# Performance work log

Hardware: AMD Instinct MI355X
Metric: run time of the kernel (lower is better)

Reference implementation:

```python
import jax, jax.numpy as jnp
import numpy as np

EPS = 1e-7  # keras.backend.epsilon()


def setup_inputs() -> dict:
    key = jax.random.key(0)
    k1, k2, k3 = jax.random.split(key, 3)
    B, N, D_in, C, D_out = 32, 2048, 8, 32, 16
    x = jax.random.normal(k1, (B, N, D_in), dtype=jnp.float32)
    W = jax.random.normal(k2, (1, N, C, D_out, D_in), dtype=jnp.float32) * 0.05
    R = jax.random.normal(k3, (1, N, C), dtype=jnp.float32)
    return {"x": x, "W": W, "R": R}


def reference(x, W, R):
    # x: [B, N, D_in]; W: [1, N, C, D_out, D_in]; R: [1, N, C]
    R_nor = jax.nn.softmax(R[0], axis=0)          # softmax over N (axis=1 of [1,N,C])
    # per-capsule transform: u[b,n,c,j] = sum_k W[n,c,j,k] * x[b,n,k]
    u = jnp.einsum('ncjk,bnk->bncj', W[0], x)
    # routing-weighted aggregation over input capsules n
    s = jnp.einsum('bncj,nc->bcj', u, R_nor)      # [B, C, D_out]
    # squash along capsule dim (original axis=-2 before squeeze == D_out)
    ss = jnp.sum(jnp.square(s), axis=-1, keepdims=True) + EPS
    scale = jnp.sqrt(ss) / (1.0 + ss)
    return scale * s                               # [B, C, D_out]
```

## Files before the change

### kernel.cpp

```cpp
#include <hip/hip_runtime.h>
#include <math.h>


#define NN 2048
#define CC 32

__device__ __forceinline__ void g2l16(const float* g, float* l) {
  __builtin_amdgcn_global_load_lds((const __attribute__((address_space(1))) void*)g,
                                   (__attribute__((address_space(3))) void*)l, 16, 0, 0);
}

__global__ void __launch_bounds__(512) caps_main(const float* __restrict__ x,
                                                 const float* __restrict__ W,
                                                 const float* __restrict__ R,
                                                 float* __restrict__ P) {
  const int bid = blockIdx.x;
  const int cq = bid >> 6;
  const int chunk = bid & 63;
  const int n0 = chunk * 32;
  const int tid = threadIdx.x;
  const int ws = tid >> 6;
  const int lane = tid & 63;
  const int j = lane & 15;
  const int bo = lane >> 4;

  extern __shared__ float smem[];
  float* ldsW = smem;
  float* ldsX = smem + 8192;
  float* red8 = smem + 4096;

#pragma unroll
  for (int it = 0; it < 2; ++it) {
    int idx = it * 512 + tid;
    int nl = idx >> 7, S = idx & 127;
    int g = S ^ (((S >> 2) ^ (S >> 4)) & 1) ^ (((S >> 3) & 1) << 1) ^ (((S >> 4) & 1) << 2);
    g2l16(W + (size_t)(n0 + nl) * 4096 + cq * 512 + g * 4,
          ldsW + (size_t)(it * 512 + ws * 64) * 4);
  }

  float4 xg[4];
  int xoff[4];
#pragma unroll
  for (int it = 0; it < 4; ++it) {
    int idx = it * 512 + tid;
    int nl = idx >> 6, r = idx & 63;
    int b = r & 31, kq = r >> 5;
    xg[it] = *(const float4*)(x + (size_t)b * (NN * 8) + (size_t)(n0 + nl) * 8 + kq * 4);
    xoff[it] = nl * 256 + kq * 128 + b;
  }
#pragma unroll
  for (int it = 0; it < 4; ++it) {
    float* d = ldsX + xoff[it];
    d[0] = xg[it].x; d[32] = xg[it].y; d[64] = xg[it].z; d[96] = xg[it].w;
  }

  float se[4] = {0.f, 0.f, 0.f, 0.f};
#pragma unroll
  for (int i = 0; i < 4; ++i) {
    int n = i * 512 + tid;
    float4 a = *(const float4*)(R + (size_t)n * CC + cq * 4);
    se[0] += expf(a.x); se[1] += expf(a.y); se[2] += expf(a.z); se[3] += expf(a.w);
  }
#pragma unroll
  for (int ci = 0; ci < 4; ++ci) {
    float v = se[ci];
#pragma unroll
    for (int d = 32; d >= 1; d >>= 1) v += __shfl_xor(v, d, 64);
    se[ci] = v;
  }
  if (lane == 0) {
#pragma unroll
    for (int ci = 0; ci < 4; ++ci) red8[ws * 4 + ci] = se[ci];
  }
  __syncthreads();

  float inv4[4];
  {
    float t[4] = {0.f, 0.f, 0.f, 0.f};
#pragma unroll
    for (int w = 0; w < 8; ++w)
#pragma unroll
      for (int ci = 0; ci < 4; ++ci) t[ci] += red8[w * 4 + ci];
#pragma unroll
    for (int ci = 0; ci < 4; ++ci) inv4[ci] = 1.0f / t[ci];
  }
  __syncthreads();

  float acc[4][8];
#pragma unroll
  for (int a = 0; a < 4; ++a)
#pragma unroll
    for (int b = 0; b < 8; ++b) acc[a][b] = 0.f;

  const int jsw = j >> 1;

#pragma unroll 1
  for (int s = 0; s < 4; ++s) {
    if (s < 3) {
      const int sb = n0 + (s + 1) * 8;
      float* wdst = ldsW + (size_t)((s + 1) & 1) * 4096;
#pragma unroll
      for (int it = 0; it < 2; ++it) {
        int idx = it * 512 + tid;
        int nl = idx >> 7, S = idx & 127;
        int g = S ^ (((S >> 2) ^ (S >> 4)) & 1) ^ (((S >> 3) & 1) << 1) ^ (((S >> 4) & 1) << 2);
        g2l16(W + (size_t)(sb + nl) * 4096 + cq * 512 + g * 4,
              wdst + (size_t)(it * 512 + ws * 64) * 4);
      }
    }
    const int n = n0 + s * 8 + ws;
    const float* Xn = ldsX + (size_t)(s * 8 + ws) * 256;
    const float* Wn = ldsW + (size_t)(s & 1) * 4096 + (size_t)ws * 512;

    const float* rr = R + (size_t)n * CC + cq * 4;
    float rv[4];
#pragma unroll
    for (int ci = 0; ci < 4; ++ci) rv[ci] = expf(rr[ci]) * inv4[ci];

#pragma unroll
    for (int kh = 0; kh < 2; ++kh) {
      float4 xlo[4], xhi[4];
#pragma unroll
      for (int kk = 0; kk < 4; ++kk) {
        const float* xp = Xn + (kh * 4 + kk) * 32 + bo * 8;
        xlo[kk] = *(const float4*)xp;
        xhi[kk] = *(const float4*)(xp + 4);
      }
#pragma unroll
      for (int ci = 0; ci < 4; ++ci) {
        int slot = (ci * 32 + j * 2 + kh) ^ jsw;
        float4 wf = *(const float4*)(Wn + slot * 4);
        float rvv = rv[ci];
        float w0 = wf.x * rvv, w1 = wf.y * rvv, w2 = wf.z * rvv, w3 = wf.w * rvv;
        float a0, a1;
#pragma unroll
        for (int bi = 0; bi < 4; ++bi) {
          a0 = acc[ci][bi];
          a0 = fmaf(w0, (&xlo[0].x)[bi], a0);
          a0 = fmaf(w1, (&xlo[1].x)[bi], a0);
          a0 = fmaf(w2, (&xlo[2].x)[bi], a0);
          a0 = fmaf(w3, (&xlo[3].x)[bi], a0);
          acc[ci][bi] = a0;
          a1 = acc[ci][bi + 4];
          a1 = fmaf(w0, (&xhi[0].x)[bi], a1);
          a1 = fmaf(w1, (&xhi[1].x)[bi], a1);
          a1 = fmaf(w2, (&xhi[2].x)[bi], a1);
          a1 = fmaf(w3, (&xhi[3].x)[bi], a1);
          acc[ci][bi + 4] = a1;
        }
      }
    }
    __syncthreads();
  }

  float* ldsAll = smem;
#pragma unroll
  for (int ci = 0; ci < 4; ++ci)
#pragma unroll
    for (int bi = 0; bi < 8; ++bi)
      ldsAll[(size_t)ws * 2048 + (ci * 8 + bi) * 64 + lane] = acc[ci][bi];
  __syncthreads();

  {
    const int t4 = tid * 4;
    float4 ssum = make_float4(0.f, 0.f, 0.f, 0.f);
#pragma unroll
    for (int w = 0; w < 8; ++w) {
      float4 v = *(const float4*)(ldsAll + (size_t)w * 2048 + t4);
      ssum.x += v.x; ssum.y += v.y; ssum.z += v.z; ssum.w += v.w;
    }
    *(float4*)(P + (size_t)bid * 2048 + t4) = ssum;
  }
}

__global__ void caps_reduce(const float* __restrict__ P, float* __restrict__ out) {
  const int g = blockIdx.x * 256 + threadIdx.x;
  const int j = g & 15;
  const int c = (g >> 4) & 31;
  const int b = g >> 9;
  const int bo = b >> 3, bi = b & 7;
  const int cq = c >> 2, ci = c & 3;
  const int idx = (ci * 8 + bi) * 64 + (bo * 16 + j);
  const float* Pq = P + (size_t)cq * 64 * 2048 + idx;

  float s = 0.f;
#pragma unroll 16
  for (int ch = 0; ch < 64; ++ch) {
    s += Pq[(size_t)ch * 2048];
  }
  float sq = s * s;
  sq += __shfl_xor(sq, 8, 16);
  sq += __shfl_xor(sq, 4, 16);
  sq += __shfl_xor(sq, 2, 16);
  sq += __shfl_xor(sq, 1, 16);
  float ss = sq + 1e-7f;
  float scale = sqrtf(ss) / (1.0f + ss);
  out[g] = scale * s;
}

extern "C" void kernel_launch(void* const* d_in, const int* in_sizes, int n_in,
                              void* d_out, int out_size, void* d_ws, size_t ws_size,
                              hipStream_t stream) {
  const float* x = (const float*)d_in[0];
  const float* W = (const float*)d_in[1];
  const float* R = (const float*)d_in[2];
  float* out = (float*)d_out;
  float* P = (float*)d_ws;

  hipFuncSetAttribute((const void*)caps_main,
                      hipFuncAttributeMaxDynamicSharedMemorySize, 65536);

  caps_main<<<512, 512, 65536, stream>>>(x, W, R, P);
  caps_reduce<<<64, 256, 0, stream>>>(P, out);
}
```

Measured before the change: 28.02 us.

## Split softmax stats into separate kernel and use per-wave W/x pipelines without block barriers

The softmax denominator is now computed once by a small caps_stats kernel instead of every block re-reading all of R and doing a block reduction. In caps_main each wave owns four consecutive n-values and loads its own W and x slices directly to LDS via global_load_lds. It double-buffers them with vmcnt waits instead of block-wide __syncthreads. This removes per-block redundant exp work and barrier stalls, at the cost of an extra kernel launch and hand-managed waitcnt ordering.

Result: faster. 26.93 us (-3.9%).

```diff
diff --git a/kernel.cpp b/kernel.cpp
--- a/kernel.cpp
+++ b/kernel.cpp
@@ -10,9 +10,26 @@
                                    (__attribute__((address_space(3))) void*)l, 16, 0, 0);
 }
 
+__global__ void caps_stats(const float* __restrict__ R, float* __restrict__ I) {
+  const int c = blockIdx.x;
+  const int t = threadIdx.x;
+  __shared__ float red[256];
+  float s = 0.f;
+#pragma unroll
+  for (int i = 0; i < 8; ++i) s += expf(R[(size_t)(t + i * 256) * CC + c]);
+  red[t] = s;
+  __syncthreads();
+  for (int h = 128; h >= 1; h >>= 1) {
+    if (t < h) red[t] += red[t + h];
+    __syncthreads();
+  }
+  if (t == 0) I[c] = 1.0f / red[0];
+}
+
 __global__ void __launch_bounds__(512) caps_main(const float* __restrict__ x,
                                                  const float* __restrict__ W,
                                                  const float* __restrict__ R,
+                                                 const float* __restrict__ I,
                                                  float* __restrict__ P) {
   const int bid = blockIdx.x;
   const int cq = bid >> 6;
@@ -27,64 +44,39 @@
   extern __shared__ float smem[];
   float* ldsW = smem;
   float* ldsX = smem + 8192;
-  float* red8 = smem + 4096;
-
-#pragma unroll
-  for (int it = 0; it < 2; ++it) {
-    int idx = it * 512 + tid;
-    int nl = idx >> 7, S = idx & 127;
-    int g = S ^ (((S >> 2) ^ (S >> 4)) & 1) ^ (((S >> 3) & 1) << 1) ^ (((S >> 4) & 1) << 2);
-    g2l16(W + (size_t)(n0 + nl) * 4096 + cq * 512 + g * 4,
-          ldsW + (size_t)(it * 512 + ws * 64) * 4);
-  }
-
-  float4 xg[4];
-  int xoff[4];
-#pragma unroll
-  for (int it = 0; it < 4; ++it) {
-    int idx = it * 512 + tid;
-    int nl = idx >> 6, r = idx & 63;
-    int b = r & 31, kq = r >> 5;
-    xg[it] = *(const float4*)(x + (size_t)b * (NN * 8) + (size_t)(n0 + nl) * 8 + kq * 4);
-    xoff[it] = nl * 256 + kq * 128 + b;
-  }
-#pragma unroll
-  for (int it = 0; it < 4; ++it) {
-    float* d = ldsX + xoff[it];
-    d[0] = xg[it].x; d[32] = xg[it].y; d[64] = xg[it].z; d[96] = xg[it].w;
-  }
-
-  float se[4] = {0.f, 0.f, 0.f, 0.f};
-#pragma unroll
-  for (int i = 0; i < 4; ++i) {
-    int n = i * 512 + tid;
-    float4 a = *(const float4*)(R + (size_t)n * CC + cq * 4);
-    se[0] += expf(a.x); se[1] += expf(a.y); se[2] += expf(a.z); se[3] += expf(a.w);
-  }
-#pragma unroll
-  for (int ci = 0; ci < 4; ++ci) {
-    float v = se[ci];
-#pragma unroll
-    for (int d = 32; d >= 1; d >>= 1) v += __shfl_xor(v, d, 64);
-    se[ci] = v;
-  }
-  if (lane == 0) {
-#pragma unroll
-    for (int ci = 0; ci < 4; ++ci) red8[ws * 4 + ci] = se[ci];
-  }
-  __syncthreads();
-
-  float inv4[4];
+  float* wW = ldsW + ws * 1024;
+  float* wX = ldsX + ws * 1024;
+  const int nw = n0 + ws * 4;
+
+  auto stageW = [&](int nl, int buf) {
+#pragma unroll
+    for (int i = 0; i < 2; ++i) {
+      int S = i * 64 + lane;
+      int g = S ^ (((S >> 2) ^ (S >> 4)) & 1) ^ (((S >> 3) & 1) << 1) ^ (((S >> 4) & 1) << 2);
+      g2l16(W + (size_t)(nw + nl) * 4096 + cq * 512 + g * 4, wW + buf * 512 + i * 256);
+    }
+  };
+  stageW(0, 0);
   {
-    float t[4] = {0.f, 0.f, 0.f, 0.f};
-#pragma unroll
-    for (int w = 0; w < 8; ++w)
-#pragma unroll
-      for (int ci = 0; ci < 4; ++ci) t[ci] += red8[w * 4 + ci];
-#pragma unroll
-    for (int ci = 0; ci < 4; ++ci) inv4[ci] = 1.0f / t[ci];
-  }
-  __syncthreads();
+    int g2 = lane ^ ((lane >> 4) << 1);
+    int b = g2 >> 1, kq = g2 & 1;
+    const float* xs = x + (size_t)b * (NN * 8) + kq * 4;
+#pragma unroll
+    for (int nl = 0; nl < 4; ++nl)
+      g2l16(xs + (size_t)(nw + nl) * 8, wX + nl * 256);
+  }
+  float rv[4][4];
+  {
+    float4 iv = *(const float4*)(I + cq * 4);
+#pragma unroll
+    for (int nl = 0; nl < 4; ++nl) {
+      float4 rq = *(const float4*)(R + (size_t)(nw + nl) * CC + cq * 4);
+      rv[nl][0] = expf(rq.x) * iv.x;
+      rv[nl][1] = expf(rq.y) * iv.y;
+      rv[nl][2] = expf(rq.z) * iv.z;
+      rv[nl][3] = expf(rq.w) * iv.w;
+    }
+  }
 
   float acc[4][8];
 #pragma unroll
@@ -94,79 +86,73 @@
 
   const int jsw = j >> 1;
 
-#pragma unroll 1
-  for (int s = 0; s < 4; ++s) {
-    if (s < 3) {
-      const int sb = n0 + (s + 1) * 8;
-      float* wdst = ldsW + (size_t)((s + 1) & 1) * 4096;
-#pragma unroll
-      for (int it = 0; it < 2; ++it) {
-        int idx = it * 512 + tid;
-        int nl = idx >> 7, S = idx & 127;
-        int g = S ^ (((S >> 2) ^ (S >> 4)) & 1) ^ (((S >> 3) & 1) << 1) ^ (((S >> 4) & 1) << 2);
-        g2l16(W + (size_t)(sb + nl) * 4096 + cq * 512 + g * 4,
-              wdst + (size_t)(it * 512 + ws * 64) * 4);
-      }
-    }
-    const int n = n0 + s * 8 + ws;
-    const float* Xn = ldsX + (size_t)(s * 8 + ws) * 256;
-    const float* Wn = ldsW + (size_t)(s & 1) * 4096 + (size_t)ws * 512;
-
-    const float* rr = R + (size_t)n * CC + cq * 4;
-    float rv[4];
-#pragma unroll
-    for (int ci = 0; ci < 4; ++ci) rv[ci] = expf(rr[ci]) * inv4[ci];
-
+  auto compute = [&](int nl, int buf) {
+    const float* Wn = wW + buf * 512;
+    const float* Xn = wX + nl * 256;
 #pragma unroll
     for (int kh = 0; kh < 2; ++kh) {
-      float4 xlo[4], xhi[4];
-#pragma unroll
-      for (int kk = 0; kk < 4; ++kk) {
-        const float* xp = Xn + (kh * 4 + kk) * 32 + bo * 8;
-        xlo[kk] = *(const float4*)xp;
-        xhi[kk] = *(const float4*)(xp + 4);
+      float4 xv[8];
+#pragma unroll
+      for (int bi = 0; bi < 8; ++bi) {
+        int G = (bo * 8 + bi) * 2 + kh;
+        int S = G ^ ((G >> 4) << 1);
+        xv[bi] = *(const float4*)(Xn + S * 4);
       }
 #pragma unroll
       for (int ci = 0; ci < 4; ++ci) {
         int slot = (ci * 32 + j * 2 + kh) ^ jsw;
         float4 wf = *(const float4*)(Wn + slot * 4);
-        float rvv = rv[ci];
+        float rvv = rv[nl][ci];
         float w0 = wf.x * rvv, w1 = wf.y * rvv, w2 = wf.z * rvv, w3 = wf.w * rvv;
-        float a0, a1;
-#pragma unroll
-        for (int bi = 0; bi < 4; ++bi) {
-          a0 = acc[ci][bi];
-          a0 = fmaf(w0, (&xlo[0].x)[bi], a0);
-          a0 = fmaf(w1, (&xlo[1].x)[bi], a0);
-          a0 = fmaf(w2, (&xlo[2].x)[bi], a0);
-          a0 = fmaf(w3, (&xlo[3].x)[bi], a0);
-          acc[ci][bi] = a0;
-          a1 = acc[ci][bi + 4];
-          a1 = fmaf(w0, (&xhi[0].x)[bi], a1);
-          a1 = fmaf(w1, (&xhi[1].x)[bi], a1);
-          a1 = fmaf(w2, (&xhi[2].x)[bi], a1);
-          a1 = fmaf(w3, (&xhi[3].x)[bi], a1);
-          acc[ci][bi + 4] = a1;
+#pragma unroll
+        for (int bi = 0; bi < 8; ++bi) {
+          float a = acc[ci][bi];
+          a = fmaf(w0, xv[bi].x, a);
+          a = fmaf(w1, xv[bi].y, a);
+          a = fmaf(w2, xv[bi].z, a);
+          a = fmaf(w3, xv[bi].w, a);
+          acc[ci][bi] = a;
         }
       }
     }
-    __syncthreads();
-  }
-
-  float* ldsAll = smem;
+  };
+
+  stageW(1, 1);
+  asm volatile("s_waitcnt vmcnt(2)" ::: "memory");
+  __builtin_amdgcn_sched_barrier(0);
+  compute(0, 0);
+  __builtin_amdgcn_sched_barrier(0);
+  stageW(2, 0);
+  asm volatile("s_waitcnt vmcnt(2)" ::: "memory");
+  __builtin_amdgcn_sched_barrier(0);
+  compute(1, 1);
+  __builtin_amdgcn_sched_barrier(0);
+  stageW(3, 1);
+  asm volatile("s_waitcnt vmcnt(2)" ::: "memory");
+  __builtin_amdgcn_sched_barrier(0);
+  compute(2, 0);
+  asm volatile("s_waitcnt vmcnt(0)" ::: "memory");
+  __builtin_amdgcn_sched_barrier(0);
+  compute(3, 1);
+
 #pragma unroll
   for (int ci = 0; ci < 4; ++ci)
 #pragma unroll
-    for (int bi = 0; bi < 8; ++bi)
-      ldsAll[(size_t)ws * 2048 + (ci * 8 + bi) * 64 + lane] = acc[ci][bi];
+    for (int bi = 0; bi < 8; ++bi) {
+      int cell = (ci * 8 + bi) * 64 + lane;
+      float* dst = (ci < 2) ? (ldsW + ws * 1024 + cell)
+                            : (ldsX + ws * 1024 + (cell - 1024));
+      *dst = acc[ci][bi];
+    }
   __syncthreads();
-
   {
     const int t4 = tid * 4;
+    const bool lo = (t4 < 1024);
     float4 ssum = make_float4(0.f, 0.f, 0.f, 0.f);
 #pragma unroll
     for (int w = 0; w < 8; ++w) {
-      float4 v = *(const float4*)(ldsAll + (size_t)w * 2048 + t4);
+      const float* src = lo ? (ldsW + w * 1024 + t4) : (ldsX + w * 1024 + (t4 - 1024));
+      float4 v = *(const float4*)src;
       ssum.x += v.x; ssum.y += v.y; ssum.z += v.z; ssum.w += v.w;
     }
     *(float4*)(P + (size_t)bid * 2048 + t4) = ssum;
@@ -205,11 +191,14 @@
   const float* W = (const float*)d_in[1];
   const float* R = (const float*)d_in[2];
   float* out = (float*)d_out;
-  float* P = (float*)d_ws;
+
+  float* I = (float*)d_ws;
+  float* P = (float*)d_ws + 64;
 
   hipFuncSetAttribute((const void*)caps_main,
                       hipFuncAttributeMaxDynamicSharedMemorySize, 65536);
 
-  caps_main<<<512, 512, 65536, stream>>>(x, W, R, P);
+  caps_stats<<<32, 256, 0, stream>>>(R, I);
+  caps_main<<<512, 512, 65536, stream>>>(x, W, R, I, P);
   caps_reduce<<<64, 256, 0, stream>>>(P, out);
 }
```
